# Kernel optimization log

Measured on AMD Instinct MI355X. Metric: run time of the kernel, lower is better.

Reference implementation:

```python
import jax, jax.numpy as jnp
import numpy as np

B, D_MODEL, D_MEM, H, N_MEM = 128, 1024, 64, 16, 4096


def setup_inputs() -> dict:
    key = jax.random.key(0)
    ks = jax.random.split(key, 6)
    scale = 1.0 / np.sqrt(D_MODEL)
    return {
        "query": jax.random.normal(ks[0], (B, D_MODEL), jnp.float32),
        "addresses": jax.random.normal(ks[1], (N_MEM, D_MEM), jnp.float32),
        "memories": jax.random.normal(ks[2], (B, N_MEM, D_MEM), jnp.float32),
        "Wq": jax.random.normal(ks[3], (D_MODEL, D_MODEL), jnp.float32) * scale,
        "bq": jnp.zeros((D_MODEL,), jnp.float32),
        "Wm": jax.random.normal(ks[4], (D_MODEL, D_MODEL), jnp.float32) * scale,
        "bm": jnp.zeros((D_MODEL,), jnp.float32),
    }


def reference(query, addresses, memories, Wq, bq, Wm, bm):
    # query projection -> heads: (B, H, d_mem)
    q = (query @ Wq.T + bq).reshape(B, H, D_MEM)
    # stage 1: build linear-attention kernel over the memory-slot dim
    k = jax.nn.relu(memories + addresses)            # (B, N, d_mem)
    matrix = jnp.einsum('bnd,bne->bde', k, memories)  # (B, d_mem, d_mem)
    normalizer = jnp.sum(k, axis=-2)                  # (B, d_mem)
    # stage 2: read the kernel with activated queries
    qa = jax.nn.relu(q)                               # (B, H, d_mem)
    numerator = jnp.einsum('bhd,bde->bhe', qa, matrix)
    denominator = jnp.einsum('bhd,bd->bh', qa, normalizer)[..., None] + 1e-5
    attn = numerator / denominator                    # (B, H, d_mem)
    return attn.reshape(B, H * D_MEM) @ Wm.T + bm     # (B, d_model)
```

## Files before the change

kernel.cpp:

```cpp
#include <hip/hip_runtime.h>
#include <hip/hip_bf16.h>

#define BATCH 128
#define DMEM 64
#define NHEAD 16
#define NMEM 4096
#define DMODEL 1024

typedef __bf16 v8bf __attribute__((ext_vector_type(8)));
typedef __bf16 v2bf __attribute__((ext_vector_type(2)));
typedef float v4f __attribute__((ext_vector_type(4)));

__device__ __forceinline__ void gemm_sk(const float* __restrict__ A,
                                        const float* __restrict__ W,
                                        const float* __restrict__ bias,
                                        float* __restrict__ C,
                                        int m0, int n0, int k0, int nchunks,
                                        float* smem) {
    float(*As)[36] = (float(*)[36])smem;
    float(*Ws)[36] = (float(*)[36])(smem + 32 * 36);
    const int t = threadIdx.x;
    const int lrow = t >> 3;
    const int lc4 = (t & 7) * 4;
    const int rp = t >> 4;
    const int cp = t & 15;

    float acc00 = 0.f, acc01 = 0.f, acc10 = 0.f, acc11 = 0.f;

    v4f av = *(const v4f*)&A[(size_t)(m0 + lrow) * DMODEL + k0 + lc4];
    v4f wv = *(const v4f*)&W[(size_t)(n0 + lrow) * DMODEL + k0 + lc4];

    for (int c = 0; c < nchunks; ++c) {
        __syncthreads();
        *(v4f*)&As[lrow][lc4] = av;
        *(v4f*)&Ws[lrow][lc4] = wv;
        __syncthreads();
        if (c + 1 < nchunks) {
            const int kc = k0 + (c + 1) * 32;
            av = *(const v4f*)&A[(size_t)(m0 + lrow) * DMODEL + kc + lc4];
            wv = *(const v4f*)&W[(size_t)(n0 + lrow) * DMODEL + kc + lc4];
        }
#pragma unroll
        for (int kk = 0; kk < 32; kk += 4) {
            v4f a0 = *(v4f*)&As[rp][kk];
            v4f a1 = *(v4f*)&As[rp + 16][kk];
            v4f b0 = *(v4f*)&Ws[cp][kk];
            v4f b1 = *(v4f*)&Ws[cp + 16][kk];
#pragma unroll
            for (int q = 0; q < 4; ++q) {
                acc00 = fmaf(a0[q], b0[q], acc00);
                acc01 = fmaf(a0[q], b1[q], acc01);
                acc10 = fmaf(a1[q], b0[q], acc10);
                acc11 = fmaf(a1[q], b1[q], acc11);
            }
        }
    }
    float bv0 = 0.f, bv1 = 0.f;
    if (bias) { bv0 = bias[n0 + cp]; bv1 = bias[n0 + cp + 16]; }
    atomicAdd(&C[(size_t)(m0 + rp) * 1024 + n0 + cp], acc00 + bv0);
    atomicAdd(&C[(size_t)(m0 + rp) * 1024 + n0 + cp + 16], acc01 + bv1);
    atomicAdd(&C[(size_t)(m0 + rp + 16) * 1024 + n0 + cp], acc10 + bv0);
    atomicAdd(&C[(size_t)(m0 + rp + 16) * 1024 + n0 + cp + 16], acc11 + bv1);
}

#define LDS_STRIDE 40

__global__ __launch_bounds__(256) void k1(const float* __restrict__ mem,
                                          const float* __restrict__ addr,
                                          float* __restrict__ pmat,
                                          float* __restrict__ pnorm,
                                          const float* __restrict__ query,
                                          const float* __restrict__ Wq,
                                          float* __restrict__ qa_ws,
                                          int S) {
    __shared__ __align__(16) char smem_raw[14336];
    const int bid = blockIdx.x;
    const int nst = BATCH * S;

    if (bid >= nst) {
        const int b2 = bid - nst;
        const int m0 = (b2 & 3) * 32;
        const int n0 = ((b2 >> 2) & 31) * 32;
        const int ks = b2 >> 7;
        gemm_sk(query, Wq, nullptr, qa_ws, m0, n0, ks * 128, 4, (float*)smem_raw);
        return;
    }

    __bf16* k_lds = (__bf16*)smem_raw;
    __bf16* m_lds = (__bf16*)(smem_raw + 5120);
    float* norm_s = (float*)(smem_raw + 10240);

    const int t = threadIdx.x;
    const int b = bid & (BATCH - 1);
    const int s = bid >> 7;
    const int slots_per = NMEM / S;
    const int chunks = slots_per >> 5;

    const int u = t & 15;
    const int v = t >> 4;
    const int d0 = u * 4;

    const int wave = t >> 6;
    const int l = t & 63;
    const int quad = l >> 4;
    const int lo = l & 15;

    const size_t mem_base = ((size_t)b * NMEM + (size_t)s * slots_per) * DMEM;
    const size_t addr_base = (size_t)s * slots_per * DMEM;
    const size_t so = (size_t)(2 * v) * DMEM + d0;

    v4f acc[4];
#pragma unroll
    for (int j = 0; j < 4; ++j) acc[j] = (v4f){0.f, 0.f, 0.f, 0.f};
    float nacc[4] = {0.f, 0.f, 0.f, 0.f};

    v4f m0v = *(const v4f*)&mem[mem_base + so];
    v4f m1v = *(const v4f*)&mem[mem_base + so + DMEM];
    v4f a0v = *(const v4f*)&addr[addr_base + so];
    v4f a1v = *(const v4f*)&addr[addr_base + so + DMEM];

    for (int c = 0; c < chunks; ++c) {
        __syncthreads();
#pragma unroll
        for (int i = 0; i < 4; ++i) {
            float kf0 = fmaxf(m0v[i] + a0v[i], 0.f);
            float kf1 = fmaxf(m1v[i] + a1v[i], 0.f);
            nacc[i] += kf0 + kf1;
            v2bf kp; kp[0] = (__bf16)kf0; kp[1] = (__bf16)kf1;
            v2bf mp; mp[0] = (__bf16)m0v[i]; mp[1] = (__bf16)m1v[i];
            *(v2bf*)&k_lds[(d0 + i) * LDS_STRIDE + 2 * v] = kp;
            *(v2bf*)&m_lds[(d0 + i) * LDS_STRIDE + 2 * v] = mp;
        }
        __syncthreads();

        if (c + 1 < chunks) {
            const size_t coff = (size_t)(c + 1) * 32 * DMEM;
            m0v = *(const v4f*)&mem[mem_base + coff + so];
            m1v = *(const v4f*)&mem[mem_base + coff + so + DMEM];
            a0v = *(const v4f*)&addr[addr_base + coff + so];
            a1v = *(const v4f*)&addr[addr_base + coff + so + DMEM];
        }

        v8bf af = *(v8bf*)&k_lds[(16 * wave + lo) * LDS_STRIDE + quad * 8];
#pragma unroll
        for (int j = 0; j < 4; ++j) {
            v8bf bf = *(v8bf*)&m_lds[(16 * j + lo) * LDS_STRIDE + quad * 8];
            acc[j] = __builtin_amdgcn_mfma_f32_16x16x32_bf16(af, bf, acc[j], 0, 0, 0);
        }
    }

#pragma unroll
    for (int j = 0; j < 4; ++j) {
#pragma unroll
        for (int r = 0; r < 4; ++r) {
            int d = 16 * wave + quad * 4 + r;
            int e = 16 * j + lo;
            pmat[(size_t)bid * 4096 + d * 64 + e] = acc[j][r];
        }
    }

#pragma unroll
    for (int i = 0; i < 4; ++i) norm_s[v * 64 + d0 + i] = nacc[i];
    __syncthreads();
    if (t < 64) {
        float sacc = 0.f;
#pragma unroll
        for (int g = 0; g < 16; ++g) sacc += norm_s[g * 64 + t];
        pnorm[(size_t)bid * 64 + t] = sacc;
    }
}

__global__ __launch_bounds__(256) void stage2(const float* __restrict__ pmat,
                                              const float* __restrict__ pnorm,
                                              const float* __restrict__ qa_raw,
                                              const float* __restrict__ bq,
                                              float* __restrict__ attn,
                                              int S) {
    __shared__ float mat_s[4096];
    __shared__ float qa_s[1024];
    __shared__ float nrm_s[64];
    const int t = threadIdx.x;
    const int b = blockIdx.x;

#pragma unroll
    for (int i = 0; i < 4; ++i) {
        const int vi = (t + 256 * i) * 4;
        v4f ssum = (v4f){0.f, 0.f, 0.f, 0.f};
        for (int s = 0; s < S; ++s) {
            v4f p = *(const v4f*)&pmat[((size_t)s * BATCH + b) * 4096 + vi];
            ssum += p;
        }
        *(v4f*)&mat_s[vi] = ssum;
    }
    if (t < 64) {
        float ssum = 0.f;
        for (int s = 0; s < S; ++s)
            ssum += pnorm[((size_t)s * BATCH + b) * 64 + t];
        nrm_s[t] = ssum;
    }
#pragma unroll
    for (int i = 0; i < 4; ++i) {
        const int idx = t + 256 * i;
        qa_s[idx] = fmaxf(qa_raw[(size_t)b * 1024 + idx] + bq[idx], 0.f);
    }
    __syncthreads();

    const int e = t & 63;
    const int hq = t >> 6;
#pragma unroll
    for (int i = 0; i < 4; ++i) {
        const int h = hq + 4 * i;
        float num = 0.f, den = 0.f;
#pragma unroll 8
        for (int d = 0; d < 64; ++d) {
            float q = qa_s[h * 64 + d];
            num = fmaf(q, mat_s[d * 64 + e], num);
            den = fmaf(q, nrm_s[d], den);
        }
        attn[(size_t)b * 1024 + h * 64 + e] = num / (den + 1e-5f);
    }
}

__global__ __launch_bounds__(256) void gemm_sk_kernel(const float* __restrict__ A,
                                                      const float* __restrict__ W,
                                                      const float* __restrict__ bias,
                                                      float* __restrict__ C) {
    __shared__ __align__(16) float smem[2 * 32 * 36];
    const int m0 = blockIdx.x * 32;
    const int n0 = blockIdx.y * 32;
    const int ks = blockIdx.z;
    gemm_sk(A, W, ks == 0 ? bias : nullptr, C, m0, n0, ks * 128, 4, smem);
}

extern "C" void kernel_launch(void* const* d_in, const int* in_sizes, int n_in,
                              void* d_out, int out_size, void* d_ws, size_t ws_size,
                              hipStream_t stream) {
    const float* query     = (const float*)d_in[0];
    const float* addresses = (const float*)d_in[1];
    const float* memories  = (const float*)d_in[2];
    const float* Wq        = (const float*)d_in[3];
    const float* bq        = (const float*)d_in[4];
    const float* Wm        = (const float*)d_in[5];
    const float* bm        = (const float*)d_in[6];
    float* out = (float*)d_out;
    float* ws = (float*)d_ws;

    int S = 8;
    while (S > 1) {
        size_t need = ((size_t)262144 + (size_t)S * (8192 + 524288)) * sizeof(float);
        if (need <= ws_size) break;
        S >>= 1;
    }

    float* qa_ws   = ws;
    float* attn_ws = ws + 131072;
    float* pnorm   = ws + 262144;
    float* pmat    = pnorm + (size_t)S * 8192;

    hipMemsetAsync(qa_ws, 0, 131072 * sizeof(float), stream);
    hipMemsetAsync(out, 0, (size_t)out_size * sizeof(float), stream);

    k1<<<dim3(BATCH * S + 1024), 256, 0, stream>>>(memories, addresses, pmat,
                                                   pnorm, query, Wq, qa_ws, S);
    stage2<<<dim3(BATCH), 256, 0, stream>>>(pmat, pnorm, qa_ws, bq, attn_ws, S);
    gemm_sk_kernel<<<dim3(4, 32, 8), 256, 0, stream>>>(attn_ws, Wm, bm, out);
}
```

Before: 260.3 us.

## Rework stage-1 kernel to 32x32x16 MFMA with double-buffered 64-slot LDS tiles

The stage-1 kernel now processes 64 memory slots per chunk instead of 32. It uses 32x32x16 bf16 MFMAs with waves split across d-strips and k-halves, and the two k-halves are reduced through LDS at the end. LDS tiles are double-buffered so each iteration needs one barrier instead of two. Threads load 8 slots of 2 columns each and write vectorised 8-wide bf16 rows, which cuts LDS write instructions and barrier stalls. The cost is more LDS (about 38 KB), more registers, and an extra cross-wave reduction. Launch bounds now request 4 blocks per CU.

```diff
diff --git a/kernel.cpp b/kernel.cpp
--- a/kernel.cpp
+++ b/kernel.cpp
@@ -3,13 +3,14 @@
 
 #define BATCH 128
 #define DMEM 64
-#define NHEAD 16
 #define NMEM 4096
 #define DMODEL 1024
+#define ROWB 72
 
 typedef __bf16 v8bf __attribute__((ext_vector_type(8)));
-typedef __bf16 v2bf __attribute__((ext_vector_type(2)));
 typedef float v4f __attribute__((ext_vector_type(4)));
+typedef float v2f __attribute__((ext_vector_type(2)));
+typedef float v16f __attribute__((ext_vector_type(16)));
 
 __device__ __forceinline__ void gemm_sk(const float* __restrict__ A,
                                         const float* __restrict__ W,
@@ -63,17 +64,15 @@
     atomicAdd(&C[(size_t)(m0 + rp + 16) * 1024 + n0 + cp + 16], acc11 + bv1);
 }
 
-#define LDS_STRIDE 40
-
-__global__ __launch_bounds__(256) void k1(const float* __restrict__ mem,
-                                          const float* __restrict__ addr,
-                                          float* __restrict__ pmat,
-                                          float* __restrict__ pnorm,
-                                          const float* __restrict__ query,
-                                          const float* __restrict__ Wq,
-                                          float* __restrict__ qa_ws,
-                                          int S) {
-    __shared__ __align__(16) char smem_raw[14336];
+__global__ __launch_bounds__(256, 4) void k1(const float* __restrict__ mem,
+                                             const float* __restrict__ addr,
+                                             float* __restrict__ pmat,
+                                             float* __restrict__ pnorm,
+                                             const float* __restrict__ query,
+                                             const float* __restrict__ Wq,
+                                             float* __restrict__ qa_ws,
+                                             int S) {
+    __shared__ __align__(16) char smem[38912];
     const int bid = blockIdx.x;
     const int nst = BATCH * S;
 
@@ -82,91 +81,110 @@
         const int m0 = (b2 & 3) * 32;
         const int n0 = ((b2 >> 2) & 31) * 32;
         const int ks = b2 >> 7;
-        gemm_sk(query, Wq, nullptr, qa_ws, m0, n0, ks * 128, 4, (float*)smem_raw);
+        gemm_sk(query, Wq, nullptr, qa_ws, m0, n0, ks * 128, 4, (float*)smem);
         return;
     }
 
-    __bf16* k_lds = (__bf16*)smem_raw;
-    __bf16* m_lds = (__bf16*)(smem_raw + 5120);
-    float* norm_s = (float*)(smem_raw + 10240);
+    float* norm_s = (float*)(smem + 36864);
 
     const int t = threadIdx.x;
+    const int g = t & 7;
+    const int d2 = t >> 3;
+    const int l = t & 63;
+    const int wv = t >> 6;
+    const int strip = wv >> 1;
+    const int kh = wv & 1;
+    const int lrow = l & 31;
+    const int lh = l >> 5;
+
     const int b = bid & (BATCH - 1);
     const int s = bid >> 7;
     const int slots_per = NMEM / S;
-    const int chunks = slots_per >> 5;
-
-    const int u = t & 15;
-    const int v = t >> 4;
-    const int d0 = u * 4;
-
-    const int wave = t >> 6;
-    const int l = t & 63;
-    const int quad = l >> 4;
-    const int lo = l & 15;
+    const int chunks = slots_per >> 6;
 
     const size_t mem_base = ((size_t)b * NMEM + (size_t)s * slots_per) * DMEM;
     const size_t addr_base = (size_t)s * slots_per * DMEM;
-    const size_t so = (size_t)(2 * v) * DMEM + d0;
-
-    v4f acc[4];
-#pragma unroll
-    for (int j = 0; j < 4; ++j) acc[j] = (v4f){0.f, 0.f, 0.f, 0.f};
-    float nacc[4] = {0.f, 0.f, 0.f, 0.f};
-
-    v4f m0v = *(const v4f*)&mem[mem_base + so];
-    v4f m1v = *(const v4f*)&mem[mem_base + so + DMEM];
-    v4f a0v = *(const v4f*)&addr[addr_base + so];
-    v4f a1v = *(const v4f*)&addr[addr_base + so + DMEM];
+    const size_t toff = (size_t)(8 * g) * DMEM + 2 * d2;
+
+    v16f acc0, acc1;
+#pragma unroll
+    for (int r = 0; r < 16; ++r) { acc0[r] = 0.f; acc1[r] = 0.f; }
+    float nacc0 = 0.f, nacc1 = 0.f;
+
+    v2f mr[8], ar[8];
+#pragma unroll
+    for (int j = 0; j < 8; ++j) {
+        mr[j] = *(const v2f*)&mem[mem_base + toff + (size_t)j * DMEM];
+        ar[j] = *(const v2f*)&addr[addr_base + toff + (size_t)j * DMEM];
+    }
 
     for (int c = 0; c < chunks; ++c) {
+        v8bf kv0, kv1, mv0, mv1;
+#pragma unroll
+        for (int j = 0; j < 8; ++j) {
+            float k0 = fmaxf(mr[j][0] + ar[j][0], 0.f);
+            float k1v = fmaxf(mr[j][1] + ar[j][1], 0.f);
+            nacc0 += k0; nacc1 += k1v;
+            kv0[j] = (__bf16)k0; kv1[j] = (__bf16)k1v;
+            mv0[j] = (__bf16)mr[j][0]; mv1[j] = (__bf16)mr[j][1];
+        }
+        if (c + 1 < chunks) {
+            const size_t coff = (size_t)(c + 1) * 64 * DMEM;
+#pragma unroll
+            for (int j = 0; j < 8; ++j) {
+                mr[j] = *(const v2f*)&mem[mem_base + coff + toff + (size_t)j * DMEM];
+                ar[j] = *(const v2f*)&addr[addr_base + coff + toff + (size_t)j * DMEM];
+            }
+        }
+        __bf16* kb = (__bf16*)(smem + (c & 1) * 18432);
+        __bf16* mb = kb + 64 * ROWB;
+        *(v8bf*)&kb[(2 * d2) * ROWB + 8 * g] = kv0;
+        *(v8bf*)&kb[(2 * d2 + 1) * ROWB + 8 * g] = kv1;
+        *(v8bf*)&mb[(2 * d2) * ROWB + 8 * g] = mv0;
+        *(v8bf*)&mb[(2 * d2 + 1) * ROWB + 8 * g] = mv1;
         __syncthreads();
-#pragma unroll
-        for (int i = 0; i < 4; ++i) {
-            float kf0 = fmaxf(m0v[i] + a0v[i], 0.f);
-            float kf1 = fmaxf(m1v[i] + a1v[i], 0.f);
-            nacc[i] += kf0 + kf1;
-            v2bf kp; kp[0] = (__bf16)kf0; kp[1] = (__bf16)kf1;
-            v2bf mp; mp[0] = (__bf16)m0v[i]; mp[1] = (__bf16)m1v[i];
-            *(v2bf*)&k_lds[(d0 + i) * LDS_STRIDE + 2 * v] = kp;
-            *(v2bf*)&m_lds[(d0 + i) * LDS_STRIDE + 2 * v] = mp;
-        }
-        __syncthreads();
-
-        if (c + 1 < chunks) {
-            const size_t coff = (size_t)(c + 1) * 32 * DMEM;
-            m0v = *(const v4f*)&mem[mem_base + coff + so];
-            m1v = *(const v4f*)&mem[mem_base + coff + so + DMEM];
-            a0v = *(const v4f*)&addr[addr_base + coff + so];
-            a1v = *(const v4f*)&addr[addr_base + coff + so + DMEM];
-        }
-
-        v8bf af = *(v8bf*)&k_lds[(16 * wave + lo) * LDS_STRIDE + quad * 8];
-#pragma unroll
-        for (int j = 0; j < 4; ++j) {
-            v8bf bf = *(v8bf*)&m_lds[(16 * j + lo) * LDS_STRIDE + quad * 8];
-            acc[j] = __builtin_amdgcn_mfma_f32_16x16x32_bf16(af, bf, acc[j], 0, 0, 0);
-        }
-    }
-
-#pragma unroll
-    for (int j = 0; j < 4; ++j) {
-#pragma unroll
-        for (int r = 0; r < 4; ++r) {
-            int d = 16 * wave + quad * 4 + r;
-            int e = 16 * j + lo;
-            pmat[(size_t)bid * 4096 + d * 64 + e] = acc[j][r];
-        }
-    }
-
-#pragma unroll
-    for (int i = 0; i < 4; ++i) norm_s[v * 64 + d0 + i] = nacc[i];
+
+        const int cb = 32 * kh + 8 * lh;
+        v8bf a0 = *(v8bf*)&kb[(32 * strip + lrow) * ROWB + cb];
+        v8bf a1 = *(v8bf*)&kb[(32 * strip + lrow) * ROWB + cb + 16];
+        v8bf b00 = *(v8bf*)&mb[lrow * ROWB + cb];
+        v8bf b01 = *(v8bf*)&mb[lrow * ROWB + cb + 16];
+        v8bf b10 = *(v8bf*)&mb[(32 + lrow) * ROWB + cb];
+        v8bf b11 = *(v8bf*)&mb[(32 + lrow) * ROWB + cb + 16];
+        acc0 = __builtin_amdgcn_mfma_f32_32x32x16_bf16(a0, b00, acc0, 0, 0, 0);
+        acc1 = __builtin_amdgcn_mfma_f32_32x32x16_bf16(a0, b10, acc1, 0, 0, 0);
+        acc0 = __builtin_amdgcn_mfma_f32_32x32x16_bf16(a1, b01, acc0, 0, 0, 0);
+        acc1 = __builtin_amdgcn_mfma_f32_32x32x16_bf16(a1, b11, acc1, 0, 0, 0);
+    }
+
     __syncthreads();
+    float* red = (float*)smem;
+    norm_s[g * 64 + 2 * d2] = nacc0;
+    norm_s[g * 64 + 2 * d2 + 1] = nacc1;
+    if (kh == 1) {
+#pragma unroll
+        for (int r = 0; r < 16; ++r) {
+            int row = (r & 3) + 8 * (r >> 2) + 4 * lh;
+            red[strip * 2048 + row * 64 + lrow] = acc0[r];
+            red[strip * 2048 + row * 64 + 32 + lrow] = acc1[r];
+        }
+    }
+    __syncthreads();
+    if (kh == 0) {
+        float* pm = pmat + (size_t)bid * 4096;
+#pragma unroll
+        for (int r = 0; r < 16; ++r) {
+            int row = (r & 3) + 8 * (r >> 2) + 4 * lh;
+            int d = 32 * strip + row;
+            pm[d * 64 + lrow] = acc0[r] + red[strip * 2048 + row * 64 + lrow];
+            pm[d * 64 + 32 + lrow] = acc1[r] + red[strip * 2048 + row * 64 + 32 + lrow];
+        }
+    }
     if (t < 64) {
-        float sacc = 0.f;
-#pragma unroll
-        for (int g = 0; g < 16; ++g) sacc += norm_s[g * 64 + t];
-        pnorm[(size_t)bid * 64 + t] = sacc;
+        float ssum = 0.f;
+#pragma unroll
+        for (int gg = 0; gg < 8; ++gg) ssum += norm_s[gg * 64 + t];
+        pnorm[(size_t)bid * 64 + t] = ssum;
     }
 }
 
```

Result: slower. 304.0 us (+16.8%).

## Double-buffer stage1 LDS, switch to 32x32 MFMA with K-split, separate Wq GEMM

Applied to the files above, without the earlier changes.

Splits the fused k1 kernel into a standalone query-projection GEMM launch followed by a dedicated stage1 kernel. Stage1 double-buffers its LDS tiles, which removes one barrier per chunk. It also replaces the 16x16x32 MFMA with 32x32x16 MFMAs, with waves splitting the K dimension and reducing partial sums through LDS at the end. The aim is fewer syncs and better MFMA efficiency, at the cost of an extra kernel launch and the loss of overlap between the Wq GEMM and the memory-bound stage1.

```diff
diff --git a/kernel.cpp b/kernel.cpp
--- a/kernel.cpp
+++ b/kernel.cpp
@@ -3,23 +3,26 @@
 
 #define BATCH 128
 #define DMEM 64
-#define NHEAD 16
 #define NMEM 4096
 #define DMODEL 1024
+#define LDS_STRIDE 40
 
 typedef __bf16 v8bf __attribute__((ext_vector_type(8)));
 typedef __bf16 v2bf __attribute__((ext_vector_type(2)));
 typedef float v4f __attribute__((ext_vector_type(4)));
-
-__device__ __forceinline__ void gemm_sk(const float* __restrict__ A,
-                                        const float* __restrict__ W,
-                                        const float* __restrict__ bias,
-                                        float* __restrict__ C,
-                                        int m0, int n0, int k0, int nchunks,
-                                        float* smem) {
+typedef float v16f __attribute__((ext_vector_type(16)));
+
+__global__ __launch_bounds__(256) void gemm_sk_kernel(const float* __restrict__ A,
+                                                      const float* __restrict__ W,
+                                                      const float* __restrict__ bias,
+                                                      float* __restrict__ C) {
+    __shared__ __align__(16) float smem[2 * 32 * 36];
     float(*As)[36] = (float(*)[36])smem;
     float(*Ws)[36] = (float(*)[36])(smem + 32 * 36);
     const int t = threadIdx.x;
+    const int m0 = blockIdx.x * 32;
+    const int n0 = blockIdx.y * 32;
+    const int k0 = blockIdx.z * 128;
     const int lrow = t >> 3;
     const int lc4 = (t & 7) * 4;
     const int rp = t >> 4;
@@ -30,12 +33,12 @@
     v4f av = *(const v4f*)&A[(size_t)(m0 + lrow) * DMODEL + k0 + lc4];
     v4f wv = *(const v4f*)&W[(size_t)(n0 + lrow) * DMODEL + k0 + lc4];
 
-    for (int c = 0; c < nchunks; ++c) {
+    for (int c = 0; c < 4; ++c) {
         __syncthreads();
         *(v4f*)&As[lrow][lc4] = av;
         *(v4f*)&Ws[lrow][lc4] = wv;
         __syncthreads();
-        if (c + 1 < nchunks) {
+        if (c + 1 < 4) {
             const int kc = k0 + (c + 1) * 32;
             av = *(const v4f*)&A[(size_t)(m0 + lrow) * DMODEL + kc + lc4];
             wv = *(const v4f*)&W[(size_t)(n0 + lrow) * DMODEL + kc + lc4];
@@ -56,41 +59,23 @@
         }
     }
     float bv0 = 0.f, bv1 = 0.f;
-    if (bias) { bv0 = bias[n0 + cp]; bv1 = bias[n0 + cp + 16]; }
+    if (bias && blockIdx.z == 0) { bv0 = bias[n0 + cp]; bv1 = bias[n0 + cp + 16]; }
     atomicAdd(&C[(size_t)(m0 + rp) * 1024 + n0 + cp], acc00 + bv0);
     atomicAdd(&C[(size_t)(m0 + rp) * 1024 + n0 + cp + 16], acc01 + bv1);
     atomicAdd(&C[(size_t)(m0 + rp + 16) * 1024 + n0 + cp], acc10 + bv0);
     atomicAdd(&C[(size_t)(m0 + rp + 16) * 1024 + n0 + cp + 16], acc11 + bv1);
 }
 
-#define LDS_STRIDE 40
-
-__global__ __launch_bounds__(256) void k1(const float* __restrict__ mem,
-                                          const float* __restrict__ addr,
-                                          float* __restrict__ pmat,
-                                          float* __restrict__ pnorm,
-                                          const float* __restrict__ query,
-                                          const float* __restrict__ Wq,
-                                          float* __restrict__ qa_ws,
-                                          int S) {
-    __shared__ __align__(16) char smem_raw[14336];
+__global__ __launch_bounds__(256, 4) void stage1(const float* __restrict__ mem,
+                                                 const float* __restrict__ addr,
+                                                 float* __restrict__ pmat,
+                                                 float* __restrict__ pnorm,
+                                                 int S) {
+    __shared__ __align__(16) char smem[24576];
+    float* norm_s = (float*)(smem + 20480);
+
+    const int t = threadIdx.x;
     const int bid = blockIdx.x;
-    const int nst = BATCH * S;
-
-    if (bid >= nst) {
-        const int b2 = bid - nst;
-        const int m0 = (b2 & 3) * 32;
-        const int n0 = ((b2 >> 2) & 31) * 32;
-        const int ks = b2 >> 7;
-        gemm_sk(query, Wq, nullptr, qa_ws, m0, n0, ks * 128, 4, (float*)smem_raw);
-        return;
-    }
-
-    __bf16* k_lds = (__bf16*)smem_raw;
-    __bf16* m_lds = (__bf16*)(smem_raw + 5120);
-    float* norm_s = (float*)(smem_raw + 10240);
-
-    const int t = threadIdx.x;
     const int b = bid & (BATCH - 1);
     const int s = bid >> 7;
     const int slots_per = NMEM / S;
@@ -100,18 +85,20 @@
     const int v = t >> 4;
     const int d0 = u * 4;
 
-    const int wave = t >> 6;
     const int l = t & 63;
-    const int quad = l >> 4;
-    const int lo = l & 15;
+    const int wv = t >> 6;
+    const int strip = wv >> 1;
+    const int kh = wv & 1;
+    const int lrow = l & 31;
+    const int lh = l >> 5;
 
     const size_t mem_base = ((size_t)b * NMEM + (size_t)s * slots_per) * DMEM;
     const size_t addr_base = (size_t)s * slots_per * DMEM;
     const size_t so = (size_t)(2 * v) * DMEM + d0;
 
-    v4f acc[4];
-#pragma unroll
-    for (int j = 0; j < 4; ++j) acc[j] = (v4f){0.f, 0.f, 0.f, 0.f};
+    v16f acc0, acc1;
+#pragma unroll
+    for (int r = 0; r < 16; ++r) { acc0[r] = 0.f; acc1[r] = 0.f; }
     float nacc[4] = {0.f, 0.f, 0.f, 0.f};
 
     v4f m0v = *(const v4f*)&mem[mem_base + so];
@@ -120,7 +107,8 @@
     v4f a1v = *(const v4f*)&addr[addr_base + so + DMEM];
 
     for (int c = 0; c < chunks; ++c) {
-        __syncthreads();
+        __bf16* kb = (__bf16*)(smem + (c & 1) * 10240);
+        __bf16* mb = kb + 64 * LDS_STRIDE;
 #pragma unroll
         for (int i = 0; i < 4; ++i) {
             float kf0 = fmaxf(m0v[i] + a0v[i], 0.f);
@@ -128,11 +116,9 @@
             nacc[i] += kf0 + kf1;
             v2bf kp; kp[0] = (__bf16)kf0; kp[1] = (__bf16)kf1;
             v2bf mp; mp[0] = (__bf16)m0v[i]; mp[1] = (__bf16)m1v[i];
-            *(v2bf*)&k_lds[(d0 + i) * LDS_STRIDE + 2 * v] = kp;
-            *(v2bf*)&m_lds[(d0 + i) * LDS_STRIDE + 2 * v] = mp;
-        }
-        __syncthreads();
-
+            *(v2bf*)&kb[(d0 + i) * LDS_STRIDE + 2 * v] = kp;
+            *(v2bf*)&mb[(d0 + i) * LDS_STRIDE + 2 * v] = mp;
+        }
         if (c + 1 < chunks) {
             const size_t coff = (size_t)(c + 1) * 32 * DMEM;
             m0v = *(const v4f*)&mem[mem_base + coff + so];
@@ -140,33 +126,44 @@
             a0v = *(const v4f*)&addr[addr_base + coff + so];
             a1v = *(const v4f*)&addr[addr_base + coff + so + DMEM];
         }
-
-        v8bf af = *(v8bf*)&k_lds[(16 * wave + lo) * LDS_STRIDE + quad * 8];
-#pragma unroll
-        for (int j = 0; j < 4; ++j) {
-            v8bf bf = *(v8bf*)&m_lds[(16 * j + lo) * LDS_STRIDE + quad * 8];
-            acc[j] = __builtin_amdgcn_mfma_f32_16x16x32_bf16(af, bf, acc[j], 0, 0, 0);
-        }
-    }
-
-#pragma unroll
-    for (int j = 0; j < 4; ++j) {
-#pragma unroll
-        for (int r = 0; r < 4; ++r) {
-            int d = 16 * wave + quad * 4 + r;
-            int e = 16 * j + lo;
-            pmat[(size_t)bid * 4096 + d * 64 + e] = acc[j][r];
-        }
-    }
-
+        __syncthreads();
+
+        const int cb = 16 * kh + 8 * lh;
+        v8bf af = *(v8bf*)&kb[(32 * strip + lrow) * LDS_STRIDE + cb];
+        v8bf b0 = *(v8bf*)&mb[lrow * LDS_STRIDE + cb];
+        v8bf b1 = *(v8bf*)&mb[(32 + lrow) * LDS_STRIDE + cb];
+        acc0 = __builtin_amdgcn_mfma_f32_32x32x16_bf16(af, b0, acc0, 0, 0, 0);
+        acc1 = __builtin_amdgcn_mfma_f32_32x32x16_bf16(af, b1, acc1, 0, 0, 0);
+    }
+
+    __syncthreads();
+    float* red = (float*)smem;
 #pragma unroll
     for (int i = 0; i < 4; ++i) norm_s[v * 64 + d0 + i] = nacc[i];
+    if (kh == 1) {
+#pragma unroll
+        for (int r = 0; r < 16; ++r) {
+            int row = (r & 3) + 8 * (r >> 2) + 4 * lh;
+            red[strip * 2048 + row * 64 + lrow] = acc0[r];
+            red[strip * 2048 + row * 64 + 32 + lrow] = acc1[r];
+        }
+    }
     __syncthreads();
+    if (kh == 0) {
+        float* pm = pmat + (size_t)bid * 4096;
+#pragma unroll
+        for (int r = 0; r < 16; ++r) {
+            int row = (r & 3) + 8 * (r >> 2) + 4 * lh;
+            int d = 32 * strip + row;
+            pm[d * 64 + lrow] = acc0[r] + red[strip * 2048 + row * 64 + lrow];
+            pm[d * 64 + 32 + lrow] = acc1[r] + red[strip * 2048 + row * 64 + 32 + lrow];
+        }
+    }
     if (t < 64) {
-        float sacc = 0.f;
-#pragma unroll
-        for (int g = 0; g < 16; ++g) sacc += norm_s[g * 64 + t];
-        pnorm[(size_t)bid * 64 + t] = sacc;
+        float ssum = 0.f;
+#pragma unroll
+        for (int g = 0; g < 16; ++g) ssum += norm_s[g * 64 + t];
+        pnorm[(size_t)bid * 64 + t] = ssum;
     }
 }
 
@@ -219,17 +216,6 @@
         }
         attn[(size_t)b * 1024 + h * 64 + e] = num / (den + 1e-5f);
     }
-}
-
-__global__ __launch_bounds__(256) void gemm_sk_kernel(const float* __restrict__ A,
-                                                      const float* __restrict__ W,
-                                                      const float* __restrict__ bias,
-                                                      float* __restrict__ C) {
-    __shared__ __align__(16) float smem[2 * 32 * 36];
-    const int m0 = blockIdx.x * 32;
-    const int n0 = blockIdx.y * 32;
-    const int ks = blockIdx.z;
-    gemm_sk(A, W, ks == 0 ? bias : nullptr, C, m0, n0, ks * 128, 4, smem);
 }
 
 extern "C" void kernel_launch(void* const* d_in, const int* in_sizes, int n_in,
@@ -260,8 +246,8 @@
     hipMemsetAsync(qa_ws, 0, 131072 * sizeof(float), stream);
     hipMemsetAsync(out, 0, (size_t)out_size * sizeof(float), stream);
 
-    k1<<<dim3(BATCH * S + 1024), 256, 0, stream>>>(memories, addresses, pmat,
-                                                   pnorm, query, Wq, qa_ws, S);
+    gemm_sk_kernel<<<dim3(4, 32, 8), 256, 0, stream>>>(query, Wq, nullptr, qa_ws);
+    stage1<<<dim3(BATCH * S), 256, 0, stream>>>(memories, addresses, pmat, pnorm, S);
     stage2<<<dim3(BATCH), 256, 0, stream>>>(pmat, pnorm, qa_ws, bq, attn_ws, S);
     gemm_sk_kernel<<<dim3(4, 32, 8), 256, 0, stream>>>(attn_ws, Wm, bm, out);
 }
```

New measurement: 283.5 us. +8.9%, slower.
